# Kernel optimization log

Measured on AMD Instinct MI355X. Metric: run time of the kernel, lower is better.

Reference implementation:

```python
import jax, jax.numpy as jnp
import numpy as np

N_SAMPLES = 32768
WINDOW = 2048
HOP = WINDOW // 2
N_FRAMES = N_SAMPLES // HOP  # 32 resonance frames
BASE_RES = 0.5
RES_SPAN = 1.0 - BASE_RES
RES_FACTOR = 0.9
N_RES = 32
EXPR = 4
CPD = 16
N_COEFFS = WINDOW // 2 + 1  # 1025


def interpolate_last_axis(x, new_size):
    # linear interpolation along last axis (align_corners=False semantics)
    old = x.shape[-1]
    pos = (jnp.arange(new_size, dtype=jnp.float32) + 0.5) * (old / new_size) - 0.5
    pos = jnp.clip(pos, 0.0, old - 1.0)
    lo = jnp.floor(pos).astype(jnp.int32)
    hi = jnp.minimum(lo + 1, old - 1)
    w = pos - lo.astype(jnp.float32)
    return x[..., lo] * (1.0 - w) + x[..., hi] * w


def overlap_add(frames):
    # frames: (..., n_frames, window); hop = window//2; output (..., n_frames*hop)
    *lead, nf, w = frames.shape
    hop = w // 2
    a = frames[..., :hop]
    b = frames[..., hop:]
    b = jnp.concatenate([jnp.zeros_like(b[..., :1, :]), b[..., :-1, :]], axis=-2)
    return (a + b).reshape(*lead, nf * hop)


def freq_domain_transfer_function_to_resonance(window_size, decay_coeffs, n_frames, start_phase, start_mags):
    # decay_coeffs/start_phase/start_mags: (nr, expr, n_coeffs); log-space decay scan
    log_decay = jnp.log(decay_coeffs + 1e-12)[..., None, :]  # (nr, expr, 1, nc)
    shape = log_decay.shape[:-2] + (n_frames, log_decay.shape[-1])
    cum = jnp.cumsum(jnp.broadcast_to(log_decay, shape), axis=-2)  # decay^(f+1)
    mags = jnp.exp(cum) * start_mags[..., None, :]
    spec = mags * jnp.exp(1j * start_phase[..., None, :])
    frames = jnp.fft.irfft(spec, n=window_size, axis=-1)  # (nr, expr, n_frames, window)
    t = jnp.arange(window_size, dtype=jnp.float32)
    hann = 0.5 - 0.5 * jnp.cos(2.0 * jnp.pi * t / window_size)
    return overlap_add(frames * hann)  # (nr, expr, n_frames*hop)


def unit_norm(x):
    return x / (jnp.linalg.norm(x, axis=-1, keepdims=True) + 1e-8)


def fft_convolve(a, b):
    n = a.shape[-1]
    fa = jnp.fft.rfft(a, n=2 * n, axis=-1)
    fb = jnp.fft.rfft(b, n=2 * n, axis=-1)
    return jnp.fft.irfft(fa * fb, n=2 * n, axis=-1)[..., :n]


def setup_inputs() -> dict:
    key = jax.random.key(0)
    ks = jax.random.split(key, 10)
    control_signal = jax.random.normal(ks[0], (2, 4, CPD, 128), dtype=jnp.float32)
    deformations = jax.random.normal(ks[1], (2, 4, EXPR, 128), dtype=jnp.float32) * 0.1
    router = jax.random.uniform(ks[2], (CPD, N_RES), minval=-1.0, maxval=1.0)

    def init_resonance(k):
        k1, k2 = jax.random.split(k)
        res = jax.random.uniform(k1, (N_RES, N_COEFFS, 1), minval=0.01, maxval=1.0)
        deform = jax.random.uniform(k2, (1, N_COEFFS, EXPR), minval=-0.02, maxval=0.02)
        return res + deform

    amp = init_resonance(ks[3])
    phase = init_resonance(ks[4])
    decay = init_resonance(ks[5])
    gains = jax.random.uniform(ks[6], (N_RES, 1), minval=0.01, maxval=1.1)
    return {"control_signal": control_signal, "deformations": deformations,
            "router": router, "amp": amp, "phase": phase, "decay": decay, "gains": gains}


def reference(control_signal, deformations, router, amp, phase, decay, gains):
    b, e, cpd, frames = control_signal.shape
    nr = router.shape[1]
    # route control plane -> resonances: (b,e,nr,frames)
    routed = jnp.einsum('becf,cr->berf', control_signal, router)
    before_upsample = routed
    # (nr, n_coeffs, expr) -> (nr, expr, n_coeffs)
    amp_t = jnp.transpose(amp, (0, 2, 1))
    phase_t = jnp.transpose(phase, (0, 2, 1))
    decay_t = jnp.transpose(decay, (0, 2, 1))
    d_coeffs = BASE_RES + jax.nn.sigmoid(decay_t) * RES_SPAN * RES_FACTOR
    res = freq_domain_transfer_function_to_resonance(
        WINDOW, d_coeffs, N_FRAMES, jnp.tanh(phase_t) * jnp.pi, jnp.abs(amp_t))
    res = unit_norm(res)[None, None]  # (1,1,nr,expr,N)
    routed_up = interpolate_last_axis(routed[:, :, :, None, :], N_SAMPLES)  # (b,e,nr,1,N)
    noise = jax.random.uniform(jax.random.key(123), routed_up.shape, minval=-1.0, maxval=1.0)
    routed_up = routed_up * noise
    conv = fft_convolve(routed_up, res)  # (b,e,nr,expr,N)
    d = deformations.at[:, :, 0, :].add(1.0)  # base deformation favors first expressivity
    d = jax.nn.softmax(d, axis=2)[:, :, None, :, :]  # (b,e,1,expr,def_frames)
    d = interpolate_last_axis(d, N_SAMPLES)
    x = jnp.sum(d * conv, axis=-2)  # mix over expressivity -> (b,e,nr,N)
    summed = jnp.tanh(x * jnp.abs(gains).reshape(1, 1, nr, 1))
    summed = jnp.sum(summed, axis=-2, keepdims=True)  # (b,e,1,N)
    return summed, before_upsample
```

## Files before the change

### kernel.cpp

```cpp
#include <hip/hip_runtime.h>
#include <hip/hip_fp16.h>
#include <stdint.h>


#define PI_F     3.14159265358979323846f
#define TWOPI_F  6.28318530717958647692f
#define UNIT64K  (TWOPI_F/65536.0f)
#define UNIT2K   (TWOPI_F/2048.0f)
#define SCALE64K (1.0f/65536.0f)
#define SKP(i)   ((i) + 4*((i) >> 4))
#define RPW 328

__device__ __forceinline__ float2 cmul(float2 a, float2 b){
  return make_float2(a.x*b.x - a.y*b.y, a.x*b.y + a.y*b.x);
}

__device__ __forceinline__ float2 twid(uint32_t e, float unit, float sign){
  float ang = (float)e * unit;
  float sn, cn;
  __sincosf(ang, &sn, &cn);
  return make_float2(cn, sign*sn);
}

__device__ __forceinline__ uint32_t rotl32(uint32_t v, int r){
  return (v << r) | (v >> (32 - r));
}

__device__ __forceinline__ void threefry2x32(uint32_t c0, uint32_t c1,
                                             uint32_t& o0, uint32_t& o1){
  const uint32_t k0 = 0u, k1 = 123u;
  const uint32_t k2 = 0x1BD11BDAu ^ k0 ^ k1;
  const uint32_t ks[3] = {k0, k1, k2};
  uint32_t x0 = c0 + k0, x1 = c1 + k1;
#pragma unroll
  for (int i = 0; i < 5; i++){
    if ((i & 1) == 0){
      x0 += x1; x1 = rotl32(x1,13); x1 ^= x0;
      x0 += x1; x1 = rotl32(x1,15); x1 ^= x0;
      x0 += x1; x1 = rotl32(x1,26); x1 ^= x0;
      x0 += x1; x1 = rotl32(x1, 6); x1 ^= x0;
    } else {
      x0 += x1; x1 = rotl32(x1,17); x1 ^= x0;
      x0 += x1; x1 = rotl32(x1,29); x1 ^= x0;
      x0 += x1; x1 = rotl32(x1,16); x1 ^= x0;
      x0 += x1; x1 = rotl32(x1,24); x1 ^= x0;
    }
    x0 += ks[(i+1)%3];
    x1 += ks[(i+2)%3] + (uint32_t)(i+1);
  }
  o0 = x0; o1 = x1;
}

__device__ __forceinline__ float jax_noise(uint32_t p){
  uint32_t b0, b1;
  threefry2x32(0u, p, b0, b1);
  uint32_t bits = b0 ^ b1;
  float u = __uint_as_float((bits >> 9) | 0x3f800000u) - 1.0f;
  return fmaxf(-1.0f, u*2.0f - 1.0f);
}

__device__ __forceinline__ void interp128(int t, int& lo, int& hi, float& w){
  float posf = ((float)t + 0.5f) * (1.0f/256.0f) - 0.5f;
  posf = fminf(fmaxf(posf, 0.0f), 127.0f);
  lo = (int)posf;
  hi = lo + 1; if (hi > 127) hi = 127;
  w = posf - (float)lo;
}

__device__ __forceinline__ __half2 u2h(uint32_t u){
  union { uint32_t u; __half2 h; } x; x.u = u; return x.h;
}
__device__ __forceinline__ uint32_t h2u(__half2 h){
  union { uint32_t u; __half2 h; } x; x.h = h; return x.u;
}
__device__ __forceinline__ constexpr int sw4(int k){ return ((k & 3) << 2) | (k >> 2); }
__device__ __forceinline__ constexpr int br4(int x){
  return ((x & 1) << 3) | ((x & 2) << 1) | ((x & 4) >> 1) | ((x & 8) >> 3);
}

__device__ __forceinline__ void cws(float2& u, const float c, const float s){
  const float x = u.x*c - u.y*s;
  u.y = u.x*s + u.y*c;
  u.x = x;
}
__device__ __forceinline__ void cwv(float2& u, const float2 w){
  const float x = u.x*w.x - u.y*w.y;
  u.y = u.x*w.y + u.y*w.x;
  u.x = x;
}

__device__ __forceinline__ void dft4(float2& a, float2& b, float2& c, float2& d,
                                     const float sgn){
  float2 t0 = make_float2(a.x + c.x, a.y + c.y);
  float2 t1 = make_float2(a.x - c.x, a.y - c.y);
  float2 t2 = make_float2(b.x + d.x, b.y + d.y);
  float2 t3 = make_float2(b.x - d.x, b.y - d.y);
  float2 i3 = make_float2(-sgn*t3.y, sgn*t3.x);
  a = make_float2(t0.x + t2.x, t0.y + t2.y);
  c = make_float2(t0.x - t2.x, t0.y - t2.y);
  b = make_float2(t1.x + i3.x, t1.y + i3.y);
  d = make_float2(t1.x - i3.x, t1.y - i3.y);
}

#define DFT16_TW(d, sgn) do { \
  const float C1_ = 0.92387953251128674f, S1_ = 0.38268343236508978f; \
  const float C2_ = 0.70710678118654752f; \
  cws(d[5],  C1_,  (sgn)*S1_); \
  cws(d[6],  C2_,  (sgn)*C2_); \
  cws(d[7],  S1_,  (sgn)*C1_); \
  cws(d[9],  C2_,  (sgn)*C2_); \
  cws(d[10], 0.0f, (sgn)); \
  cws(d[11], -C2_, (sgn)*C2_); \
  cws(d[13], S1_,  (sgn)*C1_); \
  cws(d[14], -C2_, (sgn)*C2_); \
  cws(d[15], -C1_, -(sgn)*S1_); \
} while(0)

__device__ __forceinline__ void dft16(float2* d, const float sgn){
#pragma unroll
  for (int nb = 0; nb < 4; nb++) dft4(d[nb], d[nb+4], d[nb+8], d[nb+12], sgn);
  DFT16_TW(d, sgn);
#pragma unroll
  for (int ka = 0; ka < 4; ka++) dft4(d[4*ka], d[4*ka+1], d[4*ka+2], d[4*ka+3], sgn);
}
__device__ __forceinline__ void dft16b(float2* d, const float sgn){
#pragma unroll
  for (int nb = 0; nb < 4; nb++) dft4(d[4*nb], d[4*nb+1], d[4*nb+2], d[4*nb+3], sgn);
  DFT16_TW(d, sgn);
#pragma unroll
  for (int ka = 0; ka < 4; ka++) dft4(d[ka], d[ka+4], d[ka+8], d[ka+12], sgn);
}

__device__ __forceinline__ void pass1_fwd(__half2* buf, const float2* twl, const int t){
  const int row = t >> 4, L = t & 15;
  __half2* BR = buf + row*RPW;
  float2 d[16];
#pragma unroll
  for (int H = 0; H < 16; H++) d[H] = __half22float2(BR[L + 20*H]);
  dft16(d, -1.0f);
#pragma unroll
  for (int k1 = 0; k1 < 16; k1++){
    float2 y = d[sw4(k1)];
    cwv(y, twl[(L*k1) & 255]);
    BR[L + 20*k1] = __floats2half2_rn(y.x, y.y);
  }
}

__global__ void k_routed(const float* __restrict__ ctrl, const float* __restrict__ defm,
                         const float* __restrict__ router,
                         float* __restrict__ w_routed, float* __restrict__ w_sm,
                         float* __restrict__ out1){
  int idx = blockIdx.x*blockDim.x + threadIdx.x;
  if (idx < 32768){
    int f = idx & 127, r = (idx >> 7) & 31, be = idx >> 12;
    float acc = 0.0f;
#pragma unroll
    for (int c = 0; c < 16; c++)
      acc += ctrl[(be*16 + c)*128 + f] * router[c*32 + r];
    w_routed[idx] = acc;
    out1[idx] = acc;
  } else if (idx < 32768 + 1024){
    int j = idx - 32768;
    int f = j & 127, be = j >> 7;
    float v[4];
#pragma unroll
    for (int x = 0; x < 4; x++)
      v[x] = defm[(be*4 + x)*128 + f] + (x == 0 ? 1.0f : 0.0f);
    float mx = fmaxf(fmaxf(v[0], v[1]), fmaxf(v[2], v[3]));
    float s = 0.0f;
#pragma unroll
    for (int x = 0; x < 4; x++){ v[x] = expf(v[x] - mx); s += v[x]; }
#pragma unroll
    for (int x = 0; x < 4; x++) w_sm[(be*4 + x)*128 + f] = v[x]/s;
  }
}

__global__ void k_frames(const float* __restrict__ amp, const float* __restrict__ phase,
                         const float* __restrict__ decay, float2* __restrict__ w_fr){
  const int wg = blockIdx.x;
  const int f = wg & 31;
  const int rp = wg >> 5;
  const int p = rp & 1;
  const int r = rp >> 1;
  const int t = threadIdx.x;
  __shared__ float2 buf[2048];

  for (int k = t; k <= 1024; k += 256){
    float2 S[2];
#pragma unroll
    for (int d = 0; d < 2; d++){
      const int x = 2*p + d;
      const int base = (r*1025 + k)*4 + x;
      float a  = fabsf(amp[base]);
      float ph = tanhf(phase[base]) * PI_F;
      float sg = 1.0f / (1.0f + expf(-decay[base]));
      float dc = 0.5f + 0.45f * sg;
      float mag = expf(logf(dc + 1e-12f) * (float)(f+1)) * a;
      float snv, csv;
      sincosf(ph, &snv, &csv);
      float re = mag * csv, im = mag * snv;
      if (k == 0 || k == 1024) im = 0.0f;
      S[d] = make_float2(re, im);
    }
    buf[__brev((uint32_t)k) >> 21] =
        make_float2(S[0].x - S[1].y, S[0].y + S[1].x);
    if (k >= 1 && k <= 1023)
      buf[__brev((uint32_t)(2048 - k)) >> 21] =
          make_float2(S[0].x + S[1].y, -S[0].y + S[1].x);
  }
  __syncthreads();
  for (int s = 10; s >= 0; s--){
    const int ls = 10 - s;
    const int hl = 1 << ls;
    for (int bi = t; bi < 1024; bi += 256){
      const int g = bi >> ls, j = bi & (hl - 1);
      const int i0 = g*2*hl + j, i1 = i0 + hl;
      float2 pp = buf[i0], qq = buf[i1];
      float2 w = twid((uint32_t)(j << s), UNIT2K, +1.0f);
      float2 v = cmul(qq, w);
      buf[i0] = make_float2(pp.x+v.x, pp.y+v.y);
      buf[i1] = make_float2(pp.x-v.x, pp.y-v.y);
    }
    __syncthreads();
  }
  float2* O = w_fr + (size_t)wg*2048;
  for (int u = t; u < 2048; u += 256){
    float hann = 0.5f - 0.5f*cosf(TWOPI_F * (float)u / 2048.0f);
    float sc = (1.0f/2048.0f) * hann;
    O[u] = make_float2(buf[u].x*sc, buf[u].y*sc);
  }
}

__global__ void k_ola(const float2* __restrict__ w_fr, float* __restrict__ w_resT,
                      float* __restrict__ w_sumsq){
  const int wg = blockIdx.x;
  const int cq = wg & 7;
  const int rp = wg >> 3;
  const int c0 = cq*32;
  const int r = rp >> 1, p = rp & 1;
  const int ch0 = r*4 + p*2;
  const int t = threadIdx.x;
  __shared__ float tx[32][129], ty[32][129];
  __shared__ float red[2][256];
  const float2* F = w_fr + (size_t)rp*32*2048;
  float acc0 = 0.0f, acc1 = 0.0f;
#pragma unroll
  for (int it = 0; it < 16; it++){
    const int idx = it*256 + t;
    const int cp = idx & 31, m = idx >> 5;
    const int n = c0 + cp + 256*m;
    const int f = n >> 10, u = n & 1023;
    float2 a = F[(size_t)f*2048 + u];
    float vx = a.x, vy = a.y;
    if (f > 0){
      float2 b = F[(size_t)(f-1)*2048 + u + 1024];
      vx += b.x; vy += b.y;
    }
    tx[cp][m] = vx; ty[cp][m] = vy;
    acc0 += vx*vx; acc1 += vy*vy;
  }
  red[0][t] = acc0; red[1][t] = acc1;
  __syncthreads();
#pragma unroll
  for (int it = 0; it < 16; it++){
    const int idx = it*256 + t;
    const int m = idx & 127, cp = idx >> 7;
    w_resT[(size_t)ch0*32768 + (size_t)(c0+cp)*128 + m]     = tx[cp][m];
    w_resT[(size_t)(ch0+1)*32768 + (size_t)(c0+cp)*128 + m] = ty[cp][m];
  }
  for (int off = 128; off > 0; off >>= 1){
    __syncthreads();
    if (t < off){ red[0][t] += red[0][t+off]; red[1][t] += red[1][t+off]; }
  }
  if (t == 0){
    atomicAdd(&w_sumsq[ch0],     red[0][0]);
    atomicAdd(&w_sumsq[ch0 + 1], red[1][0]);
  }
}

__global__ void k_norm(const float* __restrict__ w_sumsq, float* __restrict__ w_invnorm){
  const int s = threadIdx.x;
  if (s < 128) w_invnorm[s] = 1.0f/(sqrtf(w_sumsq[s]) + 1e-8f);
}

__global__ __launch_bounds__(256, 4)
void k_fwdA(const int mode, const float* __restrict__ w_resT,
            const float* __restrict__ w_invnorm,
            const float* __restrict__ w_routed,
            __half2* __restrict__ outh){
  const int wg = blockIdx.x;
  const int cq = wg & 15;
  const int sig = wg >> 4;
  const int t = threadIdx.x;
  const int cc = t >> 4;
  const int c  = cq*16 + cc;
  __shared__ alignas(16) __half2 buf[16*RPW];

  {
    const int mL = t & 15;
    float2 d[16];
    if (mode == 0){
      const int rr = sig >> 1, pq = sig & 1;
      const int ch0 = rr*4 + pq*2;
      const float inv0 = w_invnorm[ch0], inv1 = w_invnorm[ch0+1];
      const float* X0 = w_resT + (size_t)ch0*32768 + (size_t)c*128;
      const float* X1 = w_resT + (size_t)(ch0+1)*32768 + (size_t)c*128;
#pragma unroll
      for (int mH = 0; mH < 8; mH++){
        const int m = mL + 16*mH;
        d[mH] = make_float2(X0[m]*inv0, X1[m]*inv1);
      }
#pragma unroll
      for (int mH = 8; mH < 16; mH++) d[mH] = make_float2(0.0f, 0.0f);
    } else {
      const float* rp = w_routed + sig*128;
#pragma unroll
      for (int mH = 0; mH < 8; mH++){
        const int m = mL + 16*mH;
        const int n = c + 256*m;
        int lo, hi; float w;
        interp128(n, lo, hi, w);
        float rv = rp[lo]*(1.0f - w) + rp[hi]*w;
        d[mH] = make_float2(rv * jax_noise((uint32_t)sig*32768u + (uint32_t)n), 0.0f);
      }
#pragma unroll
      for (int mH = 8; mH < 16; mH++) d[mH] = make_float2(0.0f, 0.0f);
    }
    dft16(d, -1.0f);
    const float2 wstep = twid((uint32_t)(c + 256*mL) & 0xFFFFu, UNIT64K, -1.0f);
    float2 w = wstep;
    __half2* BR = buf + cc*RPW;
    BR[mL] = __floats2half2_rn(d[0].x, d[0].y);
#pragma unroll
    for (int rl = 1; rl < 16; rl++){
      float2 y = d[sw4(rl)];
      cwv(y, w);
      w = cmul(w, wstep);
      BR[20*rl + mL] = __floats2half2_rn(y.x, y.y);
    }
  }
  __syncthreads();
  {
    const int rl = t & 15;
    const __half2* BG = buf + cc*RPW + 20*rl;
    float2 v[16];
#pragma unroll
    for (int q4 = 0; q4 < 4; q4++){
      const uint4 ld = *reinterpret_cast<const uint4*>(BG + 4*q4);
      v[4*q4+0] = __half22float2(u2h(ld.x));
      v[4*q4+1] = __half22float2(u2h(ld.y));
      v[4*q4+2] = __half22float2(u2h(ld.z));
      v[4*q4+3] = __half22float2(u2h(ld.w));
    }
    dft16(v, -1.0f);
    const float2 wstep = twid((uint32_t)(16*c) & 0xFFFFu, UNIT64K, -1.0f);
    float2 w = wstep;
    __half2 y[16];
    y[0] = __floats2half2_rn(v[0].x, v[0].y);
#pragma unroll
    for (int rh = 1; rh < 16; rh++){
      float2 u = v[sw4(rh)];
      cwv(u, w);
      w = cmul(w, wstep);
      y[rh] = __floats2half2_rn(u.x, u.y);
    }
    uint4* O4 = reinterpret_cast<uint4*>(
        outh + (size_t)sig*65536 + (size_t)c*256 + 16*br4(rl));
#pragma unroll
    for (int q4 = 0; q4 < 4; q4++){
      uint4 st;
      st.x = h2u(y[br4(4*q4+0)]);
      st.y = h2u(y[br4(4*q4+1)]);
      st.z = h2u(y[br4(4*q4+2)]);
      st.w = h2u(y[br4(4*q4+3)]);
      O4[q4] = st;
    }
  }
}

__global__ __launch_bounds__(256, 4)
void k_fwdB(const __half2* __restrict__ spech, __half2* __restrict__ resp_t){
  const int wg = blockIdx.x;
  const int mq = wg & 15;
  const int sig = wg >> 4;
  const int m16 = mq*16;
  const int t = threadIdx.x;
  __shared__ alignas(16) __half2 buf[16*RPW];
  __shared__ float2 twl[256];
  twl[t] = twid((uint32_t)t << 8, UNIT64K, -1.0f);
  const __half2* base = spech + (size_t)sig*65536;
  {
    const int mm = t & 15, q = t >> 4;
    __half2* BR = buf + mm*RPW;
#pragma unroll
    for (int i = 0; i < 16; i++)
      BR[20*i + q] = base[(size_t)(16*i + q)*256 + m16 + mm];
  }
  __syncthreads();
  pass1_fwd(buf, twl, t);
  __syncthreads();
  {
    const int k1 = t >> 4, row = t & 15;
    __half2* BG = buf + row*RPW + 20*k1;
    float2 v[16];
#pragma unroll
    for (int cc = 0; cc < 4; cc++){
      const uint4 ld = *reinterpret_cast<const uint4*>(BG + 4*cc);
      v[4*cc+0] = __half22float2(u2h(ld.x));
      v[4*cc+1] = __half22float2(u2h(ld.y));
      v[4*cc+2] = __half22float2(u2h(ld.z));
      v[4*cc+3] = __half22float2(u2h(ld.w));
    }
    dft16(v, -1.0f);
    uint4* O4 = reinterpret_cast<uint4*>(resp_t + (((size_t)sig*16 + mq)*256 + t)*16);
#pragma unroll
    for (int cc = 0; cc < 4; cc++){
      uint4 st;
      st.x = h2u(__floats2half2_rn(v[4*cc+0].x, v[4*cc+0].y));
      st.y = h2u(__floats2half2_rn(v[4*cc+1].x, v[4*cc+1].y));
      st.z = h2u(__floats2half2_rn(v[4*cc+2].x, v[4*cc+2].y));
      st.w = h2u(__floats2half2_rn(v[4*cc+3].x, v[4*cc+3].y));
      O4[cc] = st;
    }
  }
}

__global__ __launch_bounds__(256, 4)
void k_conv(const __half2* __restrict__ ruspec,
            const __half2* __restrict__ resp_t,
            __half2* __restrict__ chunkbuf, const int gbase){
  const int wg = blockIdx.x;
  const int mq = wg & 15;
  const int p  = (wg >> 4) & 1;
  const int gl = wg >> 5;
  const int g = gbase + gl;
  const int r = g & 31;
  const int m16 = mq*16;
  const int t = threadIdx.x;
  __shared__ alignas(16) __half2 buf[16*RPW];
  __shared__ float2 twl[256];
  twl[t] = twid((uint32_t)t << 8, UNIT64K, -1.0f);

  {
    const uint4* A4 = reinterpret_cast<const uint4*>(
        ruspec + (size_t)g*65536 + (size_t)t*256 + m16);
    uint4 a0 = A4[0], a1 = A4[1], a2 = A4[2], a3 = A4[3];
    const int cs = SKP(t);
    uint32_t w[16];
    w[0]=a0.x; w[1]=a0.y; w[2]=a0.z; w[3]=a0.w;
    w[4]=a1.x; w[5]=a1.y; w[6]=a1.z; w[7]=a1.w;
    w[8]=a2.x; w[9]=a2.y; w[10]=a2.z; w[11]=a2.w;
    w[12]=a3.x; w[13]=a3.y; w[14]=a3.z; w[15]=a3.w;
#pragma unroll
    for (int mm = 0; mm < 16; mm++)
      buf[mm*RPW + cs] = u2h(w[mm]);
  }
  __syncthreads();
  pass1_fwd(buf, twl, t);
  __syncthreads();
  {
    const int k1 = t >> 4, row = t & 15;
    __half2* BG = buf + row*RPW + 20*k1;
    float2 v[16];
#pragma unroll
    for (int cc = 0; cc < 4; cc++){
      const uint4 ld = *reinterpret_cast<const uint4*>(BG + 4*cc);
      v[4*cc+0] = __half22float2(u2h(ld.x));
      v[4*cc+1] = __half22float2(u2h(ld.y));
      v[4*cc+2] = __half22float2(u2h(ld.z));
      v[4*cc+3] = __half22float2(u2h(ld.w));
    }
    const uint4* Bt = reinterpret_cast<const uint4*>(
        resp_t + (((size_t)(r*2 + p)*16 + mq)*256 + t)*16);
    uint4 b0 = Bt[0], b1 = Bt[1], b2 = Bt[2], b3 = Bt[3];
    dft16(v, -1.0f);
    uint32_t bw[16];
    bw[0]=b0.x; bw[1]=b0.y; bw[2]=b0.z; bw[3]=b0.w;
    bw[4]=b1.x; bw[5]=b1.y; bw[6]=b1.z; bw[7]=b1.w;
    bw[8]=b2.x; bw[9]=b2.y; bw[10]=b2.z; bw[11]=b2.w;
    bw[12]=b3.x; bw[13]=b3.y; bw[14]=b3.z; bw[15]=b3.w;
#pragma unroll
    for (int pp = 0; pp < 16; pp++){
      const float2 b = __half22float2(u2h(bw[pp]));
      const float zx = v[pp].x, zy = v[pp].y;
      v[pp] = make_float2((zx*b.x - zy*b.y)*SCALE64K,
                          (zx*b.y + zy*b.x)*SCALE64K);
    }
    dft16b(v, +1.0f);
    __half2 h[16];
#pragma unroll
    for (int n2 = 0; n2 < 16; n2++){
      float2 m = v[n2];
      const float2 w = twl[(n2*k1) & 255];
      const float x = m.x*w.x + m.y*w.y;
      m.y = -m.x*w.y + m.y*w.x;
      m.x = x;
      h[n2] = __floats2half2_rn(m.x, m.y);
    }
#pragma unroll
    for (int cc = 0; cc < 4; cc++){
      uint4 st;
      st.x = h2u(h[4*cc+0]);
      st.y = h2u(h[4*cc+1]);
      st.z = h2u(h[4*cc+2]);
      st.w = h2u(h[4*cc+3]);
      *reinterpret_cast<uint4*>(BG + 4*cc) = st;
    }
  }
  __syncthreads();
  {
    const int row = t >> 4, L = t & 15;
    __half2* BR = buf + row*RPW;
    float2 d[16];
#pragma unroll
    for (int k1 = 0; k1 < 16; k1++) d[k1] = __half22float2(BR[L + 20*k1]);
    dft16(d, +1.0f);
#pragma unroll
    for (int H = 0; H < 16; H++){
      const float2 x = d[sw4(H)];
      BR[L + 20*H] = __floats2half2_rn(x.x, x.y);
    }
  }
  __syncthreads();
  {
    uint4* O4 = reinterpret_cast<uint4*>(
        chunkbuf + (size_t)(gl*2 + p)*65536 + (size_t)t*256 + m16);
    const int cs = SKP(t);
#pragma unroll
    for (int q4 = 0; q4 < 4; q4++){
      uint4 st;
      st.x = h2u(buf[(4*q4+0)*RPW + cs]);
      st.y = h2u(buf[(4*q4+1)*RPW + cs]);
      st.z = h2u(buf[(4*q4+2)*RPW + cs]);
      st.w = h2u(buf[(4*q4+3)*RPW + cs]);
      O4[q4] = st;
    }
  }
}

__global__ __launch_bounds__(256, 4)
void k_invA_w(const __half2* __restrict__ chunkbuf, const int gbase,
              const float* __restrict__ w_sm, const float* __restrict__ gains,
              float* __restrict__ out0){
  const int wg = blockIdx.x;
  const int c8 = wg & 31;
  const int gl = wg >> 5;
  const int g = gbase + gl;
  const int r = g & 31, be = g >> 5;
  const int c0 = c8*8;
  const int t = threadIdx.x;
  __shared__ alignas(16) __half2 buf[16*RPW];
  __shared__ float sm_lds[512];
  sm_lds[t]       = w_sm[be*512 + t];
  sm_lds[256 + t] = w_sm[be*512 + 256 + t];

  const int row = t >> 4;
  const int p   = row >> 3;
  const int cc  = row & 7;
  const int c   = c0 + cc;
  {
    const int u = t & 15;
    const uint4* C4 = reinterpret_cast<const uint4*>(
        chunkbuf + (size_t)(gl*2 + p)*65536 + (size_t)c*256 + 16*br4(u));
    uint4 z0 = C4[0], z1 = C4[1], z2 = C4[2], z3 = C4[3];
    uint32_t zw[16];
    zw[0]=z0.x; zw[1]=z0.y; zw[2]=z0.z; zw[3]=z0.w;
    zw[4]=z1.x; zw[5]=z1.y; zw[6]=z1.z; zw[7]=z1.w;
    zw[8]=z2.x; zw[9]=z2.y; zw[10]=z2.z; zw[11]=z2.w;
    zw[12]=z3.x; zw[13]=z3.y; zw[14]=z3.z; zw[15]=z3.w;
    const float2 wstep = twid((uint32_t)(16*c) & 0xFFFFu, UNIT64K, +1.0f);
    float2 w = make_float2(1.0f, 0.0f);
    float2 d[16];
#pragma unroll
    for (int rh = 0; rh < 16; rh++){
      d[rh] = cmul(__half22float2(u2h(zw[br4(rh)])), w);
      w = cmul(w, wstep);
    }
    dft16(d, +1.0f);
    __half2* BR = buf + row*RPW;
#pragma unroll
    for (int mL = 0; mL < 16; mL++){
      const float2 s = d[sw4(mL)];
      BR[20*mL + u] = __floats2half2_rn(s.x, s.y);
    }
  }
  __syncthreads();
  const int mL = t & 15;
  float2 v[16];
  {
    const __half2* BG = buf + row*RPW + 20*mL;
#pragma unroll
    for (int q4 = 0; q4 < 4; q4++){
      const uint4 ld = *reinterpret_cast<const uint4*>(BG + 4*q4);
      v[4*q4+0] = __half22float2(u2h(ld.x));
      v[4*q4+1] = __half22float2(u2h(ld.y));
      v[4*q4+2] = __half22float2(u2h(ld.z));
      v[4*q4+3] = __half22float2(u2h(ld.w));
    }
  }
  __syncthreads();
  {
    const float2 wstep = twid((uint32_t)(c + 256*mL) & 0xFFFFu, UNIT64K, +1.0f);
    float2 w = wstep;
#pragma unroll
    for (int kL2 = 1; kL2 < 16; kL2++){
      v[kL2] = cmul(v[kL2], w);
      w = cmul(w, wstep);
    }
    dft16(v, +1.0f);
    __half2* BR = buf + row*RPW;
#pragma unroll
    for (int mH = 0; mH < 8; mH++){
      const float2 x = v[sw4(mH)];
      BR[mL + 20*mH] = __floats2half2_rn(x.x, x.y);
    }
  }
  __syncthreads();
  const float gv = fabsf(gains[r]);
#pragma unroll
  for (int it = 0; it < 4; it++){
    const int li = t + it*256;
    const int cc2 = li & 7, m = li >> 3;
    const int tt = c0 + cc2 + 256*m;
    int lo, hi; float w;
    interp128(tt, lo, hi, w);
    const int cell = (m & 15) + 20*(m >> 4);
    float2 z0 = __half22float2(buf[cc2*RPW + cell]);
    float2 z1 = __half22float2(buf[(8 + cc2)*RPW + cell]);
    float dw0 = sm_lds[0*128 + lo]*(1.0f - w) + sm_lds[0*128 + hi]*w;
    float dw1 = sm_lds[1*128 + lo]*(1.0f - w) + sm_lds[1*128 + hi]*w;
    float dw2 = sm_lds[2*128 + lo]*(1.0f - w) + sm_lds[2*128 + hi]*w;
    float dw3 = sm_lds[3*128 + lo]*(1.0f - w) + sm_lds[3*128 + hi]*w;
    float val = dw0*z0.x + dw1*z0.y + dw2*z1.x + dw3*z1.y;
    atomicAdd(&out0[(size_t)be*32768 + tt], tanhf(val*gv));
  }
}

extern "C" void kernel_launch(void* const* d_in, const int* in_sizes, int n_in,
                              void* d_out, int out_size, void* d_ws, size_t ws_size,
                              hipStream_t stream){
  const float* ctrl   = (const float*)d_in[0];
  const float* defm   = (const float*)d_in[1];
  const float* router = (const float*)d_in[2];
  const float* amp    = (const float*)d_in[3];
  const float* phase  = (const float*)d_in[4];
  const float* decay  = (const float*)d_in[5];
  const float* gains  = (const float*)d_in[6];
  float* out = (float*)d_out;
  float* ws  = (float*)d_ws;

  float*   w_resT    = ws;
  float*   w_routed  = ws + 4194304;
  float*   w_sm      = ws + 4227072;
  float*   w_invnorm = ws + 4231168;
  float*   w_sumsq   = ws + 4231296;
  __half2* ruspec_h  = (__half2*)(ws + 4231424);
  __half2* resp_h    = (__half2*)(ws + 21008640);
  __half2* chunk_h   = (__half2*)(ws + 25202944);
  const size_t base_f = 25202944;
  float2* w_fr       = (float2*)ruspec_h;
  __half2* resp_t    = (__half2*)w_resT;

  int G = 0;
  for (int gg = 128; gg >= 1; gg >>= 1){
    size_t need = (base_f + (size_t)gg*131072) * sizeof(float);
    if (need <= ws_size){ G = gg; break; }
  }

  hipMemsetAsync(d_out, 0, 262144*sizeof(float), stream);
  k_routed<<<132, 256, 0, stream>>>(ctrl, defm, router, w_routed, w_sm, out + 262144);
  if (G == 0) return;

  hipMemsetAsync(w_sumsq, 0, 128*sizeof(float), stream);
  k_frames<<<2048, 256, 0, stream>>>(amp, phase, decay, w_fr);
  k_ola<<<512, 256, 0, stream>>>(w_fr, w_resT, w_sumsq);
  k_norm<<<1, 128, 0, stream>>>(w_sumsq, w_invnorm);
  k_fwdA<<<64*16, 256, 0, stream>>>(0, w_resT, w_invnorm, w_routed, resp_h);
  k_fwdB<<<64*16, 256, 0, stream>>>(resp_h, resp_t);
  k_fwdA<<<256*16, 256, 0, stream>>>(1, w_resT, w_invnorm, w_routed, ruspec_h);
  for (int gb = 0; gb < 256; gb += G){
    k_conv<<<G*32, 256, 0, stream>>>(ruspec_h, resp_t, chunk_h, gb);
    k_invA_w<<<G*32, 256, 0, stream>>>(chunk_h, gb, w_sm, gains, out);
  }
}
```

Measured before the change: 345.0 us.

## Precompute per-coefficient spectrum params once and use LDS twiddle table in frame IFFT

```diff
diff --git a/kernel.cpp b/kernel.cpp
--- a/kernel.cpp
+++ b/kernel.cpp
@@ -175,8 +175,21 @@
   }
 }
 
-__global__ void k_frames(const float* __restrict__ amp, const float* __restrict__ phase,
-                         const float* __restrict__ decay, float2* __restrict__ w_fr){
+__global__ void k_prep(const float* __restrict__ amp, const float* __restrict__ phase,
+                       const float* __restrict__ decay, float4* __restrict__ pql){
+  const int idx = blockIdx.x*256 + threadIdx.x;
+  if (idx >= 131200) return;
+  float a  = fabsf(amp[idx]);
+  float ph = tanhf(phase[idx]) * PI_F;
+  float sg = 1.0f / (1.0f + expf(-decay[idx]));
+  float dc = 0.5f + 0.45f * sg;
+  float L  = logf(dc + 1e-12f);
+  float sn, cs;
+  sincosf(ph, &sn, &cs);
+  pql[idx] = make_float4(a*cs, a*sn, L, 0.0f);
+}
+
+__global__ void k_frames(const float4* __restrict__ pql, float2* __restrict__ w_fr){
   const int wg = blockIdx.x;
   const int f = wg & 31;
   const int rp = wg >> 5;
@@ -184,21 +197,20 @@
   const int r = rp >> 1;
   const int t = threadIdx.x;
   __shared__ float2 buf[2048];
-
+  __shared__ float2 twl2[1024];
+
+  for (int i = t; i < 1024; i += 256)
+    twl2[i] = twid((uint32_t)i, UNIT2K, +1.0f);
+
+  const float fp1 = (float)(f + 1);
   for (int k = t; k <= 1024; k += 256){
     float2 S[2];
 #pragma unroll
     for (int d = 0; d < 2; d++){
       const int x = 2*p + d;
-      const int base = (r*1025 + k)*4 + x;
-      float a  = fabsf(amp[base]);
-      float ph = tanhf(phase[base]) * PI_F;
-      float sg = 1.0f / (1.0f + expf(-decay[base]));
-      float dc = 0.5f + 0.45f * sg;
-      float mag = expf(logf(dc + 1e-12f) * (float)(f+1)) * a;
-      float snv, csv;
-      sincosf(ph, &snv, &csv);
-      float re = mag * csv, im = mag * snv;
+      const float4 q = pql[(r*1025 + k)*4 + x];
+      const float e = __expf(q.z * fp1);
+      float re = e*q.x, im = e*q.y;
       if (k == 0 || k == 1024) im = 0.0f;
       S[d] = make_float2(re, im);
     }
@@ -216,7 +228,7 @@
       const int g = bi >> ls, j = bi & (hl - 1);
       const int i0 = g*2*hl + j, i1 = i0 + hl;
       float2 pp = buf[i0], qq = buf[i1];
-      float2 w = twid((uint32_t)(j << s), UNIT2K, +1.0f);
+      float2 w = twl2[j << s];
       float2 v = cmul(qq, w);
       buf[i0] = make_float2(pp.x+v.x, pp.y+v.y);
       buf[i1] = make_float2(pp.x-v.x, pp.y-v.y);
@@ -660,9 +672,10 @@
   const size_t base_f = 25202944;
   float2* w_fr       = (float2*)ruspec_h;
   __half2* resp_t    = (__half2*)w_resT;
+  float4*  pql       = (float4*)resp_h;
 
   int G = 0;
-  for (int gg = 128; gg >= 1; gg >>= 1){
+  for (int gg = 256; gg >= 1; gg >>= 1){
     size_t need = (base_f + (size_t)gg*131072) * sizeof(float);
     if (need <= ws_size){ G = gg; break; }
   }
@@ -672,7 +685,8 @@
   if (G == 0) return;
 
   hipMemsetAsync(w_sumsq, 0, 128*sizeof(float), stream);
-  k_frames<<<2048, 256, 0, stream>>>(amp, phase, decay, w_fr);
+  k_prep<<<513, 256, 0, stream>>>(amp, phase, decay, pql);
+  k_frames<<<2048, 256, 0, stream>>>(pql, w_fr);
   k_ola<<<512, 256, 0, stream>>>(w_fr, w_resT, w_sumsq);
   k_norm<<<1, 128, 0, stream>>>(w_sumsq, w_invnorm);
   k_fwdA<<<64*16, 256, 0, stream>>>(0, w_resT, w_invnorm, w_routed, resp_h);
```

Measured after the change: 334.0 us. 3.2% less time.
